# Kernel optimization log

Measured on AMD Instinct MI355X. Metric: run time of the kernel, lower is better.

## Reference

```python
import jax, jax.numpy as jnp
import numpy as np

EMA_DECAY = 0.99
NUM_EXPERTS = 64
N_TOKENS = 2097152
TOP_K = 4


def setup_inputs() -> dict:
    key = jax.random.key(0)
    k1, k2, k3 = jax.random.split(key, 3)
    expert_indices = jax.random.randint(k1, (N_TOKENS, TOP_K), 0, NUM_EXPERTS, dtype=jnp.int64)
    expert_weights = jax.random.uniform(k2, (N_TOKENS, TOP_K), dtype=jnp.float32)
    expert_load_ema = jax.random.uniform(k3, (NUM_EXPERTS,), dtype=jnp.float32)
    expert_pair_coactivation = jnp.zeros((NUM_EXPERTS, NUM_EXPERTS), dtype=jnp.float32)
    return {
        "expert_indices": expert_indices,
        "expert_weights": expert_weights,
        "expert_load_ema": expert_load_ema,
        "expert_pair_coactivation": expert_pair_coactivation,
    }


def reference(expert_indices, expert_weights, expert_load_ema, expert_pair_coactivation):
    # expert_indices: [N, K] int; buffers: [E], [E, E]
    N, K = expert_indices.shape
    E = expert_load_ema.shape[0]

    # --- load histogram: sum over all top-k slots, normalize by N ---
    flat = expert_indices.reshape(-1)  # [N*K]
    counts = jnp.zeros((E,), dtype=expert_load_ema.dtype).at[flat].add(1.0)
    load = counts / max(N, 1)

    # EMA update of per-expert load
    new_load_ema = expert_load_ema * EMA_DECAY + load * (1.0 - EMA_DECAY)

    # --- pairwise co-activation histogram over all (k1 < k2) column pairs ---
    k1s, k2s = np.triu_indices(K, k=1)  # static pair enumeration
    a = expert_indices[:, k1s].reshape(-1)  # [N * K*(K-1)/2]
    b = expert_indices[:, k2s].reshape(-1)
    new_coact = (
        expert_pair_coactivation
        .at[a, b].add(1.0)
        .at[b, a].add(1.0)
    )

    return new_load_ema, new_coact
```

## Files before the change

### kernel.cpp

```cpp
#include <hip/hip_runtime.h>


#define N_TOKENS    2097152
#define TOP_K       4
#define NUM_EXPERTS 64
#define NCELLS      (NUM_EXPERTS * NUM_EXPERTS)

__device__ __forceinline__ void pair_add(int* s, int a, int b) {
    const int lo = min(a, b), hi = max(a, b);
    atomicAdd(&s[lo * NUM_EXPERTS + hi], 1);
}

__global__ __launch_bounds__(256) void coact_accum_kernel(
    const int* __restrict__ idx, int* __restrict__ ws)
{
    __shared__ int s_coact[NCELLS];
    for (int i = threadIdx.x; i < NCELLS; i += 256) s_coact[i] = 0;
    __syncthreads();

    const int tid    = blockIdx.x * 256 + threadIdx.x;
    const int stride = gridDim.x * 256;
    const int4* __restrict__ idx4 = (const int4*)idx;

    for (int t = tid; t < N_TOKENS; t += stride) {
        int4 v = idx4[t];
        pair_add(s_coact, v.x, v.y);
        pair_add(s_coact, v.x, v.z);
        pair_add(s_coact, v.x, v.w);
        pair_add(s_coact, v.y, v.z);
        pair_add(s_coact, v.y, v.w);
        pair_add(s_coact, v.z, v.w);
    }
    __syncthreads();

    for (int i = threadIdx.x; i < NCELLS; i += 256) {
        int v = s_coact[i];
        if (v) atomicAdd(&ws[i], v);
    }
}

__global__ __launch_bounds__(256) void finalize_kernel(
    const int* __restrict__ ws,
    const float* __restrict__ ema_in,
    const float* __restrict__ coact_in,
    float* __restrict__ out)
{
    const int t = threadIdx.x;

    for (int c = t; c < NCELLS; c += 256) {
        const int i = c >> 6, j = c & 63;
        const int lo = min(i, j), hi = max(i, j);
        int d = ws[lo * NUM_EXPERTS + hi];
        if (i == j) d *= 2;
        out[NUM_EXPERTS + c] = coact_in[c] + (float)d;
    }

    if (t < NUM_EXPERTS) {
        int rowsum = 0;
        #pragma unroll
        for (int j = 0; j < NUM_EXPERTS; ++j) {
            const int lo = min(t, j), hi = max(t, j);
            int d = ws[lo * NUM_EXPERTS + hi];
            rowsum += (j == t) ? 2 * d : d;
        }
        const int count = rowsum / 3;
        const float load = (float)count / (float)N_TOKENS;
        out[t] = ema_in[t] * 0.99f + load * 0.01f;
    }
}

extern "C" void kernel_launch(void* const* d_in, const int* in_sizes, int n_in,
                              void* d_out, int out_size, void* d_ws, size_t ws_size,
                              hipStream_t stream)
{
    const int*   idx      = (const int*)d_in[0];
    const float* ema_in   = (const float*)d_in[2];
    const float* coact_in = (const float*)d_in[3];
    float*       out      = (float*)d_out;
    int*         ws       = (int*)d_ws;

    hipMemsetAsync(ws, 0, NCELLS * sizeof(int), stream);

    coact_accum_kernel<<<512, 256, 0, stream>>>(idx, ws);
    finalize_kernel<<<1, 256, 0, stream>>>(ws, ema_in, coact_in, out);
}
```

Measured before the change: 110.7 us.

## Fuse finalize into accumulation kernel via last-block pattern and swizzle LDS bins

Merges the finalize kernel into the accumulation kernel: each block bumps a done-counter in workspace, and the last block reads the global histogram and writes the outputs. This removes a kernel launch and its gap. Shared-memory histogram indices are XOR-swizzled by the row to spread bank conflicts, with the swizzle undone on the global flush. Launch shape changes to 256 blocks of 512 threads with unroll 4. The cost is a threadfence plus a serialized final block.

```diff
diff --git a/kernel.cpp b/kernel.cpp
--- a/kernel.cpp
+++ b/kernel.cpp
@@ -2,26 +2,33 @@
 
 
 #define N_TOKENS    2097152
-#define TOP_K       4
 #define NUM_EXPERTS 64
 #define NCELLS      (NUM_EXPERTS * NUM_EXPERTS)
+#define NBLOCKS     256
+#define NTHREADS    512
 
 __device__ __forceinline__ void pair_add(int* s, int a, int b) {
     const int lo = min(a, b), hi = max(a, b);
-    atomicAdd(&s[lo * NUM_EXPERTS + hi], 1);
+    atomicAdd(&s[(lo << 6) + (hi ^ (lo & 31))], 1);
 }
 
-__global__ __launch_bounds__(256) void coact_accum_kernel(
-    const int* __restrict__ idx, int* __restrict__ ws)
+__global__ __launch_bounds__(NTHREADS) void coact_fused_kernel(
+    const int* __restrict__ idx,
+    const float* __restrict__ ema_in,
+    const float* __restrict__ coact_in,
+    int* __restrict__ ws,
+    float* __restrict__ out)
 {
     __shared__ int s_coact[NCELLS];
-    for (int i = threadIdx.x; i < NCELLS; i += 256) s_coact[i] = 0;
+    __shared__ int s_last;
+    for (int i = threadIdx.x; i < NCELLS; i += NTHREADS) s_coact[i] = 0;
     __syncthreads();
 
-    const int tid    = blockIdx.x * 256 + threadIdx.x;
-    const int stride = gridDim.x * 256;
+    const int tid    = blockIdx.x * NTHREADS + threadIdx.x;
+    const int stride = NBLOCKS * NTHREADS;
     const int4* __restrict__ idx4 = (const int4*)idx;
 
+    #pragma unroll 4
     for (int t = tid; t < N_TOKENS; t += stride) {
         int4 v = idx4[t];
         pair_add(s_coact, v.x, v.y);
@@ -33,34 +40,40 @@
     }
     __syncthreads();
 
-    for (int i = threadIdx.x; i < NCELLS; i += 256) {
+    for (int i = threadIdx.x; i < NCELLS; i += NTHREADS) {
         int v = s_coact[i];
-        if (v) atomicAdd(&ws[i], v);
+        if (v) {
+            const int lo = i >> 6;
+            const int hi = (i & 63) ^ (lo & 31);
+            atomicAdd(&ws[(lo << 6) + hi], v);
+        }
     }
-}
 
-__global__ __launch_bounds__(256) void finalize_kernel(
-    const int* __restrict__ ws,
-    const float* __restrict__ ema_in,
-    const float* __restrict__ coact_in,
-    float* __restrict__ out)
-{
-    const int t = threadIdx.x;
+    __threadfence();
+    if (threadIdx.x == 0) {
+        const int done = atomicAdd(&ws[NCELLS], 1);
+        s_last = (done == NBLOCKS - 1) ? 1 : 0;
+    }
+    __syncthreads();
+    if (!s_last) return;
 
-    for (int c = t; c < NCELLS; c += 256) {
+    __threadfence();
+
+    for (int c = threadIdx.x; c < NCELLS; c += NTHREADS) {
         const int i = c >> 6, j = c & 63;
         const int lo = min(i, j), hi = max(i, j);
-        int d = ws[lo * NUM_EXPERTS + hi];
+        int d = ws[(lo << 6) + hi];
         if (i == j) d *= 2;
         out[NUM_EXPERTS + c] = coact_in[c] + (float)d;
     }
 
-    if (t < NUM_EXPERTS) {
+    if (threadIdx.x < NUM_EXPERTS) {
+        const int t = threadIdx.x;
         int rowsum = 0;
         #pragma unroll
         for (int j = 0; j < NUM_EXPERTS; ++j) {
             const int lo = min(t, j), hi = max(t, j);
-            int d = ws[lo * NUM_EXPERTS + hi];
+            int d = ws[(lo << 6) + hi];
             rowsum += (j == t) ? 2 * d : d;
         }
         const int count = rowsum / 3;
@@ -79,8 +92,7 @@
     float*       out      = (float*)d_out;
     int*         ws       = (int*)d_ws;
 
-    hipMemsetAsync(ws, 0, NCELLS * sizeof(int), stream);
+    hipMemsetAsync(ws, 0, (NCELLS + 1) * sizeof(int), stream);
 
-    coact_accum_kernel<<<512, 256, 0, stream>>>(idx, ws);
-    finalize_kernel<<<1, 256, 0, stream>>>(ws, ema_in, coact_in, out);
+    coact_fused_kernel<<<NBLOCKS, NTHREADS, 0, stream>>>(idx, ema_in, coact_in, ws, out);
 }
```

New measurement: 133.4 us. 1.21x slower.
